# Optimization experiments

Hardware: AMD Instinct MI355X
Metric: run time of the kernel (lower is better)

The kernel has to match this reference:

```python
import jax, jax.numpy as jnp
import numpy as np

BATCH, T, H, S, P, NH = 4, 2048, 1024, 64, 64, 8
HD = H // NH

def setup_inputs() -> dict:
    key = jax.random.key(0)
    ks = jax.random.split(key, 16)
    sH = 1.0 / np.sqrt(H)
    d = {}
    d["builder_state"] = jax.random.normal(ks[0], (BATCH, T, H), jnp.float32)
    d["base_state"] = jax.random.normal(ks[1], (BATCH, T, H), jnp.float32)
    d["input_ids"] = jax.random.randint(ks[2], (BATCH, T), 0, 32000)
    d["program_probs"] = jax.random.uniform(ks[3], (BATCH, T, P), jnp.float32)
    # SSM params (scaled from raw randn for numerical stability of the 2048-step recurrence)
    d["A"] = jax.random.normal(ks[4], (S, S), jnp.float32) * (0.5 / np.sqrt(S))
    d["Bmat"] = jax.random.normal(ks[5], (H, S), jnp.float32) * sH
    d["Cmat"] = jax.random.normal(ks[6], (S, H), jnp.float32) * (1.0 / np.sqrt(S))
    d["W_in"] = jax.random.normal(ks[7], (H, H), jnp.float32) * sH
    d["b_in"] = jnp.zeros((H,), jnp.float32)
    d["W_qkv"] = jax.random.normal(ks[8], (3 * H, H), jnp.float32) * sH
    d["b_qkv"] = jnp.zeros((3 * H,), jnp.float32)
    d["W_o"] = jax.random.normal(ks[9], (H, H), jnp.float32) * sH
    d["b_o"] = jnp.zeros((H,), jnp.float32)
    d["W_prog"] = jax.random.normal(ks[10], (H, P), jnp.float32) * (1.0 / np.sqrt(P))
    d["b_prog"] = jnp.zeros((H,), jnp.float32)
    d["g1"] = jnp.ones((H,), jnp.float32); d["beta1"] = jnp.zeros((H,), jnp.float32)
    d["g2"] = jnp.ones((H,), jnp.float32); d["beta2"] = jnp.zeros((H,), jnp.float32)
    return d

def _layernorm(x, g, b):
    mu = jnp.mean(x, axis=-1, keepdims=True)
    var = jnp.mean((x - mu) ** 2, axis=-1, keepdims=True)
    return (x - mu) * jax.lax.rsqrt(var + 1e-5) * g + b

def _mha(q_in, kv_in, W_qkv, b_qkv, W_o, b_o):
    Wq, Wk, Wv = jnp.split(W_qkv, 3, axis=0)
    bq, bk, bv = jnp.split(b_qkv, 3, axis=0)
    def heads(x, W, b):  # [B,T,H] -> [B,NH,T,HD]
        y = x @ W.T + b
        return y.reshape(y.shape[0], y.shape[1], NH, HD).transpose(0, 2, 1, 3)
    q, k, v = heads(q_in, Wq, bq), heads(kv_in, Wk, bk), heads(kv_in, Wv, bv)
    scores = jnp.einsum('bhqd,bhkd->bhqk', q, k) * (1.0 / np.sqrt(HD))
    attn = jax.nn.softmax(scores, axis=-1)
    out = jnp.einsum('bhqk,bhkd->bhqd', attn, v)
    out = out.transpose(0, 2, 1, 3).reshape(q_in.shape)
    return out @ W_o.T + b_o

def reference(builder_state, base_state, input_ids, program_probs,
              A, Bmat, Cmat, W_in, b_in, W_qkv, b_qkv, W_o, b_o,
              W_prog, b_prog, g1, beta1, g2, beta2):
    # cross-attention sublayer (norm1 shared between builder and base states)
    residual = builder_state
    x = _layernorm(builder_state, g1, beta1)
    base_n = _layernorm(base_state, g1, beta1)
    x = residual + _mha(x, base_n, W_qkv, b_qkv, W_o, b_o)
    # SSM sublayer: state_{t} = silu(A @ state_{t-1}) + B^T u_t ; y_t = state_t @ C
    residual = x
    xn = _layernorm(x, g2, beta2)
    U = (xn @ W_in.T + b_in) @ Bmat            # [B,T,S] precomputed input drive
    def step(s, u_t):                           # s: [B,S], u_t: [B,S]
        s = jax.nn.silu(s @ A.T) + u_t
        return s, s
    _, states = jax.lax.scan(step, jnp.zeros((builder_state.shape[0], S), U.dtype),
                             U.transpose(1, 0, 2))  # states: [T,B,S]
    ssm_out = jnp.einsum('tbs,sh->bth', states, Cmat)
    x = residual + ssm_out
    # program modulation
    mod = program_probs.mean(axis=1) @ W_prog.T + b_prog   # [B,H]
    return x + mod[:, None, :]
```

## Files before the change

### kernel.cpp

```cpp
#include <hip/hip_runtime.h>
#include <cstdint>
#include <cstddef>

typedef unsigned short u16;
typedef short bf16x8 __attribute__((ext_vector_type(8)));
typedef float f32x4 __attribute__((ext_vector_type(4)));
typedef u16 u16x4 __attribute__((ext_vector_type(4)));
typedef u16 u16x8 __attribute__((ext_vector_type(8)));

#define DEVFN static __device__ __forceinline__

DEVFN u16 f32_to_bf16(float f){
  unsigned u = __float_as_uint(f);
  u += 0x7fffu + ((u >> 16) & 1u);
  return (u16)(u >> 16);
}

DEVFN f32x4 mfma16(bf16x8 a, bf16x8 b, f32x4 c){
  return __builtin_amdgcn_mfma_f32_16x16x32_bf16(a, b, c, 0, 0, 0);
}

DEVFN void gload_lds16(const void* g, void* l){
  __builtin_amdgcn_global_load_lds(
      (const __attribute__((address_space(1))) void*)g,
      (__attribute__((address_space(3))) void*)l, 16, 0, 0);
}

__global__ __launch_bounds__(256,1) void prep_kernel(
    const float* __restrict__ W_qkv, const float* __restrict__ W_o,
    const float* __restrict__ Cm, const float* __restrict__ W_in,
    const float* __restrict__ Bm, const float* __restrict__ b_in,
    u16* __restrict__ Wq16, u16* __restrict__ Wo16, u16* __restrict__ CmT,
    u16* __restrict__ WcT, float* __restrict__ ub)
{
  const int blk = blockIdx.x;
  if (blk < 1024){
    for (int i = blk*256 + threadIdx.x; i < 786432; i += 1024*256){
      float4 v = ((const float4*)W_qkv)[i];
      u16x4 o; o[0]=f32_to_bf16(v.x); o[1]=f32_to_bf16(v.y); o[2]=f32_to_bf16(v.z); o[3]=f32_to_bf16(v.w);
      ((u16x4*)Wq16)[i] = o;
    }
  } else if (blk < 1280){
    for (int i = (blk-1024)*256 + threadIdx.x; i < 262144; i += 256*256){
      float4 v = ((const float4*)W_o)[i];
      u16x4 o; o[0]=f32_to_bf16(v.x); o[1]=f32_to_bf16(v.y); o[2]=f32_to_bf16(v.z); o[3]=f32_to_bf16(v.w);
      ((u16x4*)Wo16)[i] = o;
    }
  } else if (blk < 1536){
    int i = (blk-1280)*256 + threadIdx.x;
    int h = i >> 6, s = i & 63;
    CmT[i] = f32_to_bf16(Cm[s*1024 + h]);
  } else if (blk < 1792){
    int b2 = blk - 1536;
    const int kl = threadIdx.x & 63, sl = threadIdx.x >> 6;
    const int k = ((b2 & 15) << 6) + kl;
    const int s = ((b2 >> 4) << 2) + sl;
    float a = 0.f;
#pragma unroll 8
    for (int jj = 0; jj < 1024; jj++) a = fmaf(W_in[jj*1024 + k], Bm[jj*64 + s], a);
    WcT[s*1024 + k] = f32_to_bf16(a);
  } else {
    if (threadIdx.x < 64){
      const int s = threadIdx.x;
      float a = 0.f;
      for (int jj = 0; jj < 1024; jj++) a = fmaf(b_in[jj], Bm[jj*64 + s], a);
      ub[s] = a;
    }
  }
}

DEVFN void ln_row(const float* __restrict__ srcrow, u16* __restrict__ dstrow,
                  const float* __restrict__ g, const float* __restrict__ beta, int t)
{
  const float4 v = ((const float4*)srcrow)[t];
  float s1 = v.x+v.y+v.z+v.w;
  float s2 = v.x*v.x+v.y*v.y+v.z*v.z+v.w*v.w;
#pragma unroll
  for (int off = 32; off > 0; off >>= 1){ s1 += __shfl_xor(s1, off); s2 += __shfl_xor(s2, off); }
  __shared__ float w1[4], w2[4];
  if ((t & 63) == 0){ w1[t>>6] = s1; w2[t>>6] = s2; }
  __syncthreads();
  s1 = (w1[0]+w1[1])+(w1[2]+w1[3]);
  s2 = (w2[0]+w2[1])+(w2[2]+w2[3]);
  const float mean = s1*(1.f/1024.f);
  const float var  = s2*(1.f/1024.f) - mean*mean;
  const float rstd = rsqrtf(var + 1e-5f);
  const float4 gv = ((const float4*)g)[t];
  const float4 bv = ((const float4*)beta)[t];
  u16x4 o;
  o[0] = f32_to_bf16((v.x-mean)*rstd*gv.x + bv.x);
  o[1] = f32_to_bf16((v.y-mean)*rstd*gv.y + bv.y);
  o[2] = f32_to_bf16((v.z-mean)*rstd*gv.z + bv.z);
  o[3] = f32_to_bf16((v.w-mean)*rstd*gv.w + bv.w);
  *(u16x4*)&dstrow[t*4] = o;
}

__global__ __launch_bounds__(256,1) void ln_bf16_kernel(
    const float* __restrict__ src, u16* __restrict__ dst,
    const float* __restrict__ g, const float* __restrict__ beta)
{
  const int row = blockIdx.x;
  ln_row(src + (size_t)row*1024, dst + (size_t)row*1024, g, beta, threadIdx.x);
}

__global__ __launch_bounds__(256,1) void ln2x_bf16_kernel(
    const float* __restrict__ src0, u16* __restrict__ dst0,
    const float* __restrict__ src1, u16* __restrict__ dst1,
    const float* __restrict__ g, const float* __restrict__ beta)
{
  int row = blockIdx.x;
  if (row < 8192) ln_row(src0 + (size_t)row*1024, dst0 + (size_t)row*1024, g, beta, threadIdx.x);
  else { row -= 8192; ln_row(src1 + (size_t)row*1024, dst1 + (size_t)row*1024, g, beta, threadIdx.x); }
}

template<int BM,int BN,int WM,int WN,int MT,int NT,int EPI>
__global__ __launch_bounds__(256,1) void gemm_bt(
    const u16* __restrict__ Ag, const u16* __restrict__ Bg,
    void* __restrict__ Cout, const float* __restrict__ bias,
    const float* __restrict__ resid, const float* __restrict__ modv,
    int M, int N, int K)
{
  static_assert(BM == WM*MT*16 && BN == WN*NT*16 && WM*WN == 4, "tile config");
  __shared__ u16 As[BM*32];
  __shared__ u16 Bs[BN*32];
  const int t = threadIdx.x;
  const int lane = t & 63, wave = t >> 6;
  const int wm = wave / WN, wn = wave % WN;
  const int lrow = lane & 15, lq = lane >> 4;
  const int m0 = blockIdx.y * BM, n0 = blockIdx.x * BN;

  f32x4 acc[MT][NT];
#pragma unroll
  for (int i = 0; i < MT; i++)
#pragma unroll
    for (int j = 0; j < NT; j++){ acc[i][j][0]=0.f; acc[i][j][1]=0.f; acc[i][j][2]=0.f; acc[i][j][3]=0.f; }

  const int sA = lq ^ (lrow & 3);

  for (int kt = 0; kt < K; kt += 32){
#pragma unroll
    for (int i = 0; i < BM/64; i++){
      int idx = (i*4 + wave)*64 + lane;
      int r = idx >> 2, s = idx & 3;
      int c = s ^ (r & 3);
      gload_lds16(&Ag[(size_t)(m0 + r)*K + kt + c*8], &As[(size_t)(i*4 + wave)*64*8]);
    }
#pragma unroll
    for (int i = 0; i < BN/64; i++){
      int idx = (i*4 + wave)*64 + lane;
      int r = idx >> 2, s = idx & 3;
      int c = s ^ (r & 3);
      gload_lds16(&Bg[(size_t)(n0 + r)*K + kt + c*8], &Bs[(size_t)(i*4 + wave)*64*8]);
    }
    __syncthreads();
    bf16x8 af[MT], bfr[NT];
#pragma unroll
    for (int mt = 0; mt < MT; mt++)
      af[mt] = *(const bf16x8*)&As[(wm*MT*16 + mt*16 + lrow)*32 + sA*8];
#pragma unroll
    for (int nt = 0; nt < NT; nt++)
      bfr[nt] = *(const bf16x8*)&Bs[(wn*NT*16 + nt*16 + lrow)*32 + sA*8];
#pragma unroll
    for (int mt = 0; mt < MT; mt++)
#pragma unroll
      for (int nt = 0; nt < NT; nt++)
        acc[mt][nt] = mfma16(af[mt], bfr[nt], acc[mt][nt]);
    __syncthreads();
  }
  const int rb = m0 + wm*MT*16;
  const int cb = n0 + wn*NT*16;
#pragma unroll
  for (int mt = 0; mt < MT; mt++){
#pragma unroll
    for (int nt = 0; nt < NT; nt++){
#pragma unroll
      for (int r = 0; r < 4; r++){
        int row = rb + mt*16 + lq*4 + r;
        int col = cb + nt*16 + lrow;
        float v = acc[mt][nt][r];
        if (EPI & 2) v += bias[col];
        if (EPI & 16) v *= (0.08838834764831845f * 1.4426950408889634f);
        if (EPI & 4) v += resid[(size_t)row*N + col];
        if (EPI & 8) v += modv[(row >> 11)*1024 + col];
        if (EPI & 1) ((u16*)Cout)[(size_t)row*N + col] = f32_to_bf16(v);
        else         ((float*)Cout)[(size_t)row*N + col] = v;
      }
    }
  }
}

__global__ __launch_bounds__(512,1) void flash_attn(
    const u16* __restrict__ Qb, const u16* __restrict__ KVb, u16* __restrict__ Ob)
{
  __shared__ u16 Ks[64*128];
  __shared__ unsigned Vt2[128*34];
  __shared__ u16 Ps[8][16*68];
  const int t = threadIdx.x;
  const int lane = t & 63, wave = t >> 6;
  const int lrow = lane & 15, lq = lane >> 4;
  const int b = blockIdx.y >> 3, h = blockIdx.y & 7;
  const int q0 = blockIdx.x * 128;

  bf16x8 qf[4];
  {
    int grow = b*2048 + q0 + wave*16 + lrow;
#pragma unroll
    for (int ks = 0; ks < 4; ks++)
      qf[ks] = *(const bf16x8*)&Qb[(size_t)grow*1024 + h*128 + ks*32 + lq*8];
  }
  float lsum[4] = {0.f,0.f,0.f,0.f};
  f32x4 Oa[8];
#pragma unroll
  for (int i = 0; i < 8; i++){ Oa[i][0]=0.f; Oa[i][1]=0.f; Oa[i][2]=0.f; Oa[i][3]=0.f; }

  const int key_k = t >> 3, cg = t & 7;
  const int kp = t & 31, dg = t >> 5;

  const size_t KSTEP = (size_t)64*2048;
  const u16* Kpg = &KVb[(size_t)(b*2048 + key_k)*2048 + h*128];
  const u16* Vpg = &KVb[(size_t)(b*2048 + kp*2)*2048 + h*128 + 1024 + dg*8];

  u16x8 kreg[2];
  u16x8 vreg[2];

#pragma unroll
  for (int i = 0; i < 2; i++) kreg[i] = *(const u16x8*)&Kpg[(cg*2+i)*8];
  vreg[0] = *(const u16x8*)&Vpg[0];
  vreg[1] = *(const u16x8*)&Vpg[2048];
#pragma unroll
  for (int i = 0; i < 2; i++){
    int ch = cg*2 + i;
    int ph = ch ^ (key_k & 7);
    *(u16x8*)&Ks[key_k*128 + ph*8] = kreg[i];
  }
#pragma unroll
  for (int jj = 0; jj < 8; jj++)
    Vt2[(dg*8+jj)*34 + kp] = (unsigned)vreg[0][jj] | ((unsigned)vreg[1][jj] << 16);

  for (int kt = 0; kt < 32; kt++){
    __syncthreads();
    if (kt < 31){
      const u16* kpg = Kpg + (size_t)(kt+1)*KSTEP;
#pragma unroll
      for (int i = 0; i < 2; i++) kreg[i] = *(const u16x8*)&kpg[(cg*2+i)*8];
      const u16* vg = Vpg + (size_t)(kt+1)*KSTEP;
      vreg[0] = *(const u16x8*)&vg[0];
      vreg[1] = *(const u16x8*)&vg[2048];
    }

    f32x4 sacc[4];
    __builtin_amdgcn_s_setprio(1);
#pragma unroll
    for (int nt = 0; nt < 4; nt++){
      f32x4 a; a[0]=0.f; a[1]=0.f; a[2]=0.f; a[3]=0.f;
#pragma unroll
      for (int ks = 0; ks < 4; ks++){
        int ph = (ks*4 + lq) ^ (lrow & 7);
        bf16x8 kf = *(const bf16x8*)&Ks[(nt*16+lrow)*128 + ph*8];
        a = mfma16(qf[ks], kf, a);
      }
      sacc[nt] = a;
    }
    __builtin_amdgcn_s_setprio(0);
#pragma unroll
    for (int nt = 0; nt < 4; nt++)
#pragma unroll
      for (int r = 0; r < 4; r++){
        float p = exp2f(sacc[nt][r]);
        lsum[r] += p;
        Ps[wave][(lq*4+r)*68 + nt*16 + lrow] = f32_to_bf16(p);
      }
    __builtin_amdgcn_s_setprio(1);
#pragma unroll
    for (int ks2 = 0; ks2 < 2; ks2++){
      bf16x8 pa;
      ((u16x4*)&pa)[0] = *(const u16x4*)&Ps[wave][lrow*68 + ks2*32 + lq*8];
      ((u16x4*)&pa)[1] = *(const u16x4*)&Ps[wave][lrow*68 + ks2*32 + lq*8 + 4];
#pragma unroll
      for (int nt2 = 0; nt2 < 8; nt2++){
        bf16x8 vf;
        int dwoff = (nt2*16+lrow)*34 + ks2*16 + lq*4;
        ((uint2*)&vf)[0] = *(const uint2*)&Vt2[dwoff];
        ((uint2*)&vf)[1] = *(const uint2*)&Vt2[dwoff+2];
        Oa[nt2] = mfma16(pa, vf, Oa[nt2]);
      }
    }
    __builtin_amdgcn_s_setprio(0);
    __syncthreads();
    if (kt < 31){
#pragma unroll
      for (int i = 0; i < 2; i++){
        int ch = cg*2 + i;
        int ph = ch ^ (key_k & 7);
        *(u16x8*)&Ks[key_k*128 + ph*8] = kreg[i];
      }
#pragma unroll
      for (int jj = 0; jj < 8; jj++)
        Vt2[(dg*8+jj)*34 + kp] = (unsigned)vreg[0][jj] | ((unsigned)vreg[1][jj] << 16);
    }
  }
#pragma unroll
  for (int r = 0; r < 4; r++){
#pragma unroll
    for (int off = 1; off < 16; off <<= 1) lsum[r] += __shfl_xor(lsum[r], off);
  }
  float inv[4];
#pragma unroll
  for (int r = 0; r < 4; r++) inv[r] = 1.0f / lsum[r];
  const int growb = b*2048 + q0 + wave*16;
#pragma unroll
  for (int nt2 = 0; nt2 < 8; nt2++)
#pragma unroll
    for (int r = 0; r < 4; r++){
      float o = Oa[nt2][r]*inv[r];
      Ob[(size_t)(growb + lq*4 + r)*1024 + h*128 + nt2*16 + lrow] = f32_to_bf16(o);
    }
}

__global__ __launch_bounds__(64,1) void scan_chunk_kernel(
    const float* __restrict__ U, const float* __restrict__ A, u16* __restrict__ S)
{
  const int b = blockIdx.y, c = blockIdx.x, j = threadIdx.x;
  float Ar[64];
#pragma unroll
  for (int k = 0; k < 64; k++) Ar[k] = A[j*64 + k];
  const float* Ub = U + (size_t)b*2048*64;
  u16* Sb = S + (size_t)b*2048*64;
  const int tout = c*32;
  const int tend = tout + 32;
  int t0 = tout - 48; if (t0 < 0) t0 = 0;
  __shared__ float sbuf[2][64];
  sbuf[0][j] = 0.f;
  __syncthreads();
  float unext = Ub[t0*64 + j];
  const float NLOG2E = -1.4426950408889634f;
  for (int t = t0; t < tend; t++){
    const int cur = (t - t0) & 1;
    f32x4 sv[16];
#pragma unroll
    for (int r = 0; r < 16; r++) sv[r] = *((const f32x4*)&sbuf[cur][r*4]);
    float u = unext;
    int tn = t + 1; if (tn >= tend) tn = tend - 1;
    unext = Ub[tn*64 + j];
    float a0=0.f, a1=0.f, a2=0.f, a3=0.f;
#pragma unroll
    for (int r = 0; r < 16; r++){
      a0 = fmaf(Ar[4*r+0], sv[r][0], a0);
      a1 = fmaf(Ar[4*r+1], sv[r][1], a1);
      a2 = fmaf(Ar[4*r+2], sv[r][2], a2);
      a3 = fmaf(Ar[4*r+3], sv[r][3], a3);
    }
    float y = (a0+a1)+(a2+a3);
    float e = exp2f(y*NLOG2E);
    float s = fmaf(y, __builtin_amdgcn_rcpf(1.f + e), u);
    sbuf[cur^1][j] = s;
    if (t >= tout) Sb[t*64 + j] = f32_to_bf16(s);
  }
}

__global__ __launch_bounds__(256,1) void pmean1_kernel(const float* __restrict__ pp,
                                                       float* __restrict__ partial){
  const int c = blockIdx.x, b = blockIdx.y, t = threadIdx.x;
  const int p = t & 63, g = t >> 6;
  const float* basep = pp + (size_t)b*2048*64 + (size_t)c*64*64;
  float s = 0.f;
#pragma unroll
  for (int i = g*16; i < g*16 + 16; i++) s += basep[i*64 + p];
  __shared__ float red[256];
  red[t] = s;
  __syncthreads();
  if (t < 64) partial[(b*32 + c)*64 + t] = (red[t] + red[64+t]) + (red[128+t] + red[192+t]);
}

__global__ __launch_bounds__(256,1) void pmean2_mod_kernel(
    const float* __restrict__ partial, const float* __restrict__ Wp,
    const float* __restrict__ bp, float* __restrict__ mo)
{
  const int b = blockIdx.x, t = threadIdx.x;
  const int p = t & 63, g = t >> 6;
  float s = 0.f;
#pragma unroll
  for (int c = g*8; c < g*8 + 8; c++) s += partial[(b*32 + c)*64 + p];
  __shared__ float red[256];
  __shared__ float pms[64];
  red[t] = s;
  __syncthreads();
  if (t < 64) pms[t] = ((red[t] + red[64+t]) + (red[128+t] + red[192+t])) * (1.f/2048.f);
  __syncthreads();
#pragma unroll
  for (int j = 0; j < 4; j++){
    int hc = t*4 + j;
    float a = bp[hc];
#pragma unroll 8
    for (int q = 0; q < 64; q++) a = fmaf(pms[q], Wp[hc*64+q], a);
    mo[b*1024 + hc] = a;
  }
}

extern "C" void kernel_launch(void* const* d_in, const int* in_sizes, int n_in,
                              void* d_out, int out_size, void* d_ws, size_t ws_size,
                              hipStream_t stream)
{
  (void)in_sizes; (void)n_in; (void)out_size; (void)ws_size;
  const float* builder = (const float*)d_in[0];
  const float* base    = (const float*)d_in[1];
  const float* pp      = (const float*)d_in[3];
  const float* Amat    = (const float*)d_in[4];
  const float* Bmat    = (const float*)d_in[5];
  const float* Cmat    = (const float*)d_in[6];
  const float* W_in    = (const float*)d_in[7];
  const float* b_in    = (const float*)d_in[8];
  const float* W_qkv   = (const float*)d_in[9];
  const float* b_qkv   = (const float*)d_in[10];
  const float* W_o     = (const float*)d_in[11];
  const float* b_o     = (const float*)d_in[12];
  const float* W_prog  = (const float*)d_in[13];
  const float* b_prog  = (const float*)d_in[14];
  const float* g1      = (const float*)d_in[15];
  const float* beta1   = (const float*)d_in[16];
  const float* g2      = (const float*)d_in[17];
  const float* beta2   = (const float*)d_in[18];
  float* out = (float*)d_out;

  char* ws = (char*)d_ws;
  const size_t MB = (size_t)1 << 20;
  u16*   Qb   = (u16*)  (ws + 0*MB);
  u16*   KVb  = (u16*)  (ws + 16*MB);
  float* Xf   = (float*)(ws + 48*MB);
  u16*   QN   = (u16*)  (ws + 80*MB);
  u16*   KVN  = (u16*)  (ws + 96*MB);
  u16*   Wq16 = (u16*)  (ws + 112*MB);
  u16*   Wo16 = (u16*)  (ws + 118*MB);
  u16*   WcT  = (u16*)  (ws + 120*MB);
  u16*   CmT  = (u16*)  (ws + 120*MB + 256*1024);
  float* Uf   = (float*)(ws + 121*MB);
  u16*   Sb   = (u16*)  (ws + 123*MB);
  float* ub   = (float*)(ws + 124*MB);
  float* modv = (float*)(ws + 124*MB + 8192);
  float* ppart= (float*)(ws + 124*MB + 32768);

  prep_kernel<<<1793,256,0,stream>>>(W_qkv, W_o, Cmat, W_in, Bmat, b_in,
                                     Wq16, Wo16, CmT, WcT, ub);

  ln2x_bf16_kernel<<<16384,256,0,stream>>>(builder, QN, base, KVN, g1, beta1);

  gemm_bt<128,128,2,2,4,4,19><<<dim3(8,64),256,0,stream>>>(QN,  Wq16,              Qb,  b_qkv,      nullptr, nullptr, 8192,1024,1024);
  gemm_bt<128,128,2,2,4,4,3><<<dim3(16,64),256,0,stream>>>(KVN, Wq16 + 1024*1024, KVb, b_qkv+1024, nullptr, nullptr, 8192,2048,1024);

  flash_attn<<<dim3(16,32),512,0,stream>>>(Qb, KVb, QN);

  gemm_bt<128,128,2,2,4,4,6><<<dim3(8,64),256,0,stream>>>(QN, Wo16, Xf, b_o, builder, nullptr, 8192,1024,1024);

  ln_bf16_kernel<<<8192,256,0,stream>>>(Xf, KVN, g2, beta2);

  gemm_bt<64,64,2,2,2,2,2><<<dim3(1,128),256,0,stream>>>(KVN, WcT, Uf, ub, nullptr, nullptr, 8192,64,1024);

  scan_chunk_kernel<<<dim3(64,4),64,0,stream>>>(Uf, Amat, Sb);

  pmean1_kernel<<<dim3(32,4),256,0,stream>>>(pp, ppart);
  pmean2_mod_kernel<<<4,256,0,stream>>>(ppart, W_prog, b_prog, modv);

  gemm_bt<128,128,2,2,4,4,12><<<dim3(8,64),256,0,stream>>>(Sb, CmT, out, nullptr, Xf, modv, 8192,1024,64);
}
```

Before: 545.8 us.

## Merge Q and KV projection GEMMs and fold small reductions into existing kernels

The two separate Q and KV projection GEMMs become one launch of 1536 blocks that picks operands per block, which removes a launch and fills the GPU better. The program-probs partial means move into extra blocks of prep_kernel, and the final modulation reduction moves into an extra column of blocks in the scan kernel, removing two small launches. The output-projection GEMM also switches to 256x128 tiles. One risk is that the 64-thread modulation blocks, which loop over 16 outputs, could lengthen the scan's critical path.

```diff
diff --git a/kernel.cpp b/kernel.cpp
--- a/kernel.cpp
+++ b/kernel.cpp
@@ -30,8 +30,9 @@
     const float* __restrict__ W_qkv, const float* __restrict__ W_o,
     const float* __restrict__ Cm, const float* __restrict__ W_in,
     const float* __restrict__ Bm, const float* __restrict__ b_in,
+    const float* __restrict__ pp,
     u16* __restrict__ Wq16, u16* __restrict__ Wo16, u16* __restrict__ CmT,
-    u16* __restrict__ WcT, float* __restrict__ ub)
+    u16* __restrict__ WcT, float* __restrict__ ub, float* __restrict__ partial)
 {
   const int blk = blockIdx.x;
   if (blk < 1024){
@@ -59,13 +60,25 @@
 #pragma unroll 8
     for (int jj = 0; jj < 1024; jj++) a = fmaf(W_in[jj*1024 + k], Bm[jj*64 + s], a);
     WcT[s*1024 + k] = f32_to_bf16(a);
-  } else {
+  } else if (blk == 1792){
     if (threadIdx.x < 64){
       const int s = threadIdx.x;
       float a = 0.f;
       for (int jj = 0; jj < 1024; jj++) a = fmaf(b_in[jj], Bm[jj*64 + s], a);
       ub[s] = a;
     }
+  } else {
+    const int idx = blk - 1793;
+    const int c = idx & 31, b = idx >> 5, t = threadIdx.x;
+    const int p = t & 63, g = t >> 6;
+    const float* basep = pp + (size_t)b*2048*64 + (size_t)c*64*64;
+    float s = 0.f;
+#pragma unroll
+    for (int i = g*16; i < g*16 + 16; i++) s += basep[i*64 + p];
+    __shared__ float red[256];
+    red[t] = s;
+    __syncthreads();
+    if (t < 64) partial[(b*32 + c)*64 + t] = (red[t] + red[64+t]) + (red[128+t] + red[192+t]);
   }
 }
 
@@ -179,11 +192,91 @@
         int col = cb + nt*16 + lrow;
         float v = acc[mt][nt][r];
         if (EPI & 2) v += bias[col];
-        if (EPI & 16) v *= (0.08838834764831845f * 1.4426950408889634f);
         if (EPI & 4) v += resid[(size_t)row*N + col];
         if (EPI & 8) v += modv[(row >> 11)*1024 + col];
         if (EPI & 1) ((u16*)Cout)[(size_t)row*N + col] = f32_to_bf16(v);
         else         ((float*)Cout)[(size_t)row*N + col] = v;
+      }
+    }
+  }
+}
+
+__global__ __launch_bounds__(256,1) void gemm_qkv(
+    const u16* __restrict__ QNa, const u16* __restrict__ KVNa,
+    const u16* __restrict__ Wq, u16* __restrict__ Qb, u16* __restrict__ KVb,
+    const float* __restrict__ bias)
+{
+  const int bid = blockIdx.x;
+  const u16* Ag; const u16* Bg; u16* Cout; const float* bp;
+  int N, m0, n0; float scale;
+  if (bid < 512){
+    Ag = QNa; Bg = Wq; Cout = Qb; bp = bias; N = 1024;
+    m0 = (bid >> 3) * 128; n0 = (bid & 7) * 128;
+    scale = 0.08838834764831845f * 1.4426950408889634f;
+  } else {
+    int b2 = bid - 512;
+    Ag = KVNa; Bg = Wq + 1024*1024; Cout = KVb; bp = bias + 1024; N = 2048;
+    m0 = (b2 >> 4) * 128; n0 = (b2 & 15) * 128;
+    scale = 1.0f;
+  }
+  const int K = 1024;
+  __shared__ u16 As[128*32];
+  __shared__ u16 Bs[128*32];
+  const int t = threadIdx.x;
+  const int lane = t & 63, wave = t >> 6;
+  const int wm = wave >> 1, wn = wave & 1;
+  const int lrow = lane & 15, lq = lane >> 4;
+
+  f32x4 acc[4][4];
+#pragma unroll
+  for (int i = 0; i < 4; i++)
+#pragma unroll
+    for (int j = 0; j < 4; j++){ acc[i][j][0]=0.f; acc[i][j][1]=0.f; acc[i][j][2]=0.f; acc[i][j][3]=0.f; }
+
+  const int sA = lq ^ (lrow & 3);
+
+  for (int kt = 0; kt < K; kt += 32){
+#pragma unroll
+    for (int i = 0; i < 2; i++){
+      int idx = (i*4 + wave)*64 + lane;
+      int r = idx >> 2, s = idx & 3;
+      int c = s ^ (r & 3);
+      gload_lds16(&Ag[(size_t)(m0 + r)*K + kt + c*8], &As[(size_t)(i*4 + wave)*64*8]);
+    }
+#pragma unroll
+    for (int i = 0; i < 2; i++){
+      int idx = (i*4 + wave)*64 + lane;
+      int r = idx >> 2, s = idx & 3;
+      int c = s ^ (r & 3);
+      gload_lds16(&Bg[(size_t)(n0 + r)*K + kt + c*8], &Bs[(size_t)(i*4 + wave)*64*8]);
+    }
+    __syncthreads();
+    bf16x8 af[4], bfr[4];
+#pragma unroll
+    for (int mt = 0; mt < 4; mt++)
+      af[mt] = *(const bf16x8*)&As[(wm*64 + mt*16 + lrow)*32 + sA*8];
+#pragma unroll
+    for (int nt = 0; nt < 4; nt++)
+      bfr[nt] = *(const bf16x8*)&Bs[(wn*64 + nt*16 + lrow)*32 + sA*8];
+#pragma unroll
+    for (int mt = 0; mt < 4; mt++)
+#pragma unroll
+      for (int nt = 0; nt < 4; nt++)
+        acc[mt][nt] = mfma16(af[mt], bfr[nt], acc[mt][nt]);
+    __syncthreads();
+  }
+  const int rb = m0 + wm*64;
+  const int cb = n0 + wn*64;
+#pragma unroll
+  for (int mt = 0; mt < 4; mt++){
+#pragma unroll
+    for (int nt = 0; nt < 4; nt++){
+#pragma unroll
+      for (int r = 0; r < 4; r++){
+        int row = rb + mt*16 + lq*4 + r;
+        int col = cb + nt*16 + lrow;
+        float v = (acc[mt][nt][r] + bp[col]) * scale;
+        Cout[(size_t)row*N + col] = f32_to_bf16(v);
       }
     }
   }
@@ -318,9 +411,27 @@
 }
 
 __global__ __launch_bounds__(64,1) void scan_chunk_kernel(
-    const float* __restrict__ U, const float* __restrict__ A, u16* __restrict__ S)
+    const float* __restrict__ U, const float* __restrict__ A, u16* __restrict__ S,
+    const float* __restrict__ partial, const float* __restrict__ Wp,
+    const float* __restrict__ bp, float* __restrict__ mo)
 {
   const int b = blockIdx.y, c = blockIdx.x, j = threadIdx.x;
+  if (c == 64){
+    float s = 0.f;
+#pragma unroll
+    for (int cc = 0; cc < 32; cc++) s += partial[(b*32 + cc)*64 + j];
+    __shared__ float pms[64];
+    pms[j] = s * (1.f/2048.f);
+    __syncthreads();
+    for (int jo = 0; jo < 16; jo++){
+      int hc = jo*64 + j;
+      float a = bp[hc];
+#pragma unroll 8
+      for (int q = 0; q < 64; q++) a = fmaf(pms[q], Wp[hc*64+q], a);
+      mo[b*1024 + hc] = a;
+    }
+    return;
+  }
   float Ar[64];
 #pragma unroll
   for (int k = 0; k < 64; k++) Ar[k] = A[j*64 + k];
@@ -355,45 +466,6 @@
     float s = fmaf(y, __builtin_amdgcn_rcpf(1.f + e), u);
     sbuf[cur^1][j] = s;
     if (t >= tout) Sb[t*64 + j] = f32_to_bf16(s);
-  }
-}
-
-__global__ __launch_bounds__(256,1) void pmean1_kernel(const float* __restrict__ pp,
-                                                       float* __restrict__ partial){
-  const int c = blockIdx.x, b = blockIdx.y, t = threadIdx.x;
-  const int p = t & 63, g = t >> 6;
-  const float* basep = pp + (size_t)b*2048*64 + (size_t)c*64*64;
-  float s = 0.f;
-#pragma unroll
-  for (int i = g*16; i < g*16 + 16; i++) s += basep[i*64 + p];
-  __shared__ float red[256];
-  red[t] = s;
-  __syncthreads();
-  if (t < 64) partial[(b*32 + c)*64 + t] = (red[t] + red[64+t]) + (red[128+t] + red[192+t]);
-}
-
-__global__ __launch_bounds__(256,1) void pmean2_mod_kernel(
-    const float* __restrict__ partial, const float* __restrict__ Wp,
-    const float* __restrict__ bp, float* __restrict__ mo)
-{
-  const int b = blockIdx.x, t = threadIdx.x;
-  const int p = t & 63, g = t >> 6;
-  float s = 0.f;
-#pragma unroll
-  for (int c = g*8; c < g*8 + 8; c++) s += partial[(b*32 + c)*64 + p];
-  __shared__ float red[256];
-  __shared__ float pms[64];
-  red[t] = s;
-  __syncthreads();
-  if (t < 64) pms[t] = ((red[t] + red[64+t]) + (red[128+t] + red[192+t])) * (1.f/2048.f);
-  __syncthreads();
-#pragma unroll
-  for (int j = 0; j < 4; j++){
-    int hc = t*4 + j;
-    float a = bp[hc];
-#pragma unroll 8
-    for (int q = 0; q < 64; q++) a = fmaf(pms[q], Wp[hc*64+q], a);
-    mo[b*1024 + hc] = a;
   }
 }
 
@@ -439,26 +511,22 @@
   float* modv = (float*)(ws + 124*MB + 8192);
   float* ppart= (float*)(ws + 124*MB + 32768);
 
-  prep_kernel<<<1793,256,0,stream>>>(W_qkv, W_o, Cmat, W_in, Bmat, b_in,
-                                     Wq16, Wo16, CmT, WcT, ub);
+  prep_kernel<<<1921,256,0,stream>>>(W_qkv, W_o, Cmat, W_in, Bmat, b_in, pp,
+                                     Wq16, Wo16, CmT, WcT, ub, ppart);
 
   ln2x_bf16_kernel<<<16384,256,0,stream>>>(builder, QN, base, KVN, g1, beta1);
 
-  gemm_bt<128,128,2,2,4,4,19><<<dim3(8,64),256,0,stream>>>(QN,  Wq16,              Qb,  b_qkv,      nullptr, nullptr, 8192,1024,1024);
-  gemm_bt<128,128,2,2,4,4,3><<<dim3(16,64),256,0,stream>>>(KVN, Wq16 + 1024*1024, KVb, b_qkv+1024, nullptr, nullptr, 8192,2048,1024);
+  gemm_qkv<<<1536,256,0,stream>>>(QN, KVN, Wq16, Qb, KVb, b_qkv);
 
   flash_attn<<<dim3(16,32),512,0,stream>>>(Qb, KVb, QN);
 
-  gemm_bt<128,128,2,2,4,4,6><<<dim3(8,64),256,0,stream>>>(QN, Wo16, Xf, b_o, builder, nullptr, 8192,1024,1024);
+  gemm_bt<256,128,2,2,8,4,6><<<dim3(8,32),256,0,stream>>>(QN, Wo16, Xf, b_o, builder, nullptr, 8192,1024,1024);
 
   ln_bf16_kernel<<<8192,256,0,stream>>>(Xf, KVN, g2, beta2);
 
   gemm_bt<64,64,2,2,2,2,2><<<dim3(1,128),256,0,stream>>>(KVN, WcT, Uf, ub, nullptr, nullptr, 8192,64,1024);
 
-  scan_chunk_kernel<<<dim3(64,4),64,0,stream>>>(Uf, Amat, Sb);
-
-  pmean1_kernel<<<dim3(32,4),256,0,stream>>>(pp, ppart);
-  pmean2_mod_kernel<<<4,256,0,stream>>>(ppart, W_prog, b_prog, modv);
+  scan_chunk_kernel<<<dim3(65,4),64,0,stream>>>(Uf, Amat, Sb, ppart, W_prog, b_prog, modv);
 
   gemm_bt<128,128,2,2,4,4,12><<<dim3(8,64),256,0,stream>>>(Sb, CmT, out, nullptr, Xf, modv, 8192,1024,64);
 }
```

Measured after the change: 542.5 us. No clear change (-0.6%).
